# Kernel optimization log

Measured on AMD Instinct MI355X. Metric: run time of the kernel, lower is better.

The kernel has to match this reference:

```python
import jax, jax.numpy as jnp
import numpy as np

FEATURE_DIM = 2048
CROP_PE_DIM = 96
FULL = FEATURE_DIM + CROP_PE_DIM  # 2144
H1 = 1024
H2 = 512
NEG_SLOPE = 0.01


def leaky(x):
    return jnp.where(x >= 0, x, NEG_SLOPE * x)


def setup_inputs() -> dict:
    key = jax.random.key(0)
    ks = jax.random.split(key, 8)
    B, T = 512, 32
    features = jax.random.normal(ks[0], (B, T, FULL), dtype=jnp.float32)

    def lin(k, fan_in, fan_out):
        kw, kb = jax.random.split(k)
        bound = 1.0 / np.sqrt(fan_in)
        W = jax.random.uniform(kw, (fan_in, fan_out), minval=-bound, maxval=bound, dtype=jnp.float32)
        b = jax.random.uniform(kb, (fan_out,), minval=-bound, maxval=bound, dtype=jnp.float32)
        return W, b

    We, be = lin(ks[1], 2 * FULL, H1)
    W1a, b1a = lin(ks[2], H1, H1)
    W1b, b1b = lin(ks[3], H1, H2)
    W2a, b2a = lin(ks[4], H2, H2)
    W2b, b2b = lin(ks[5], H2, H2)
    Wd, bd = lin(ks[6], H2, 3)
    return {
        "features": features,
        "We": We, "be": be,
        "W1a": W1a, "b1a": b1a, "W1b": W1b, "b1b": b1b,
        "W2a": W2a, "b2a": b2a, "W2b": W2b, "b2b": b2b,
        "Wd": Wd, "bd": bd,
    }


def reference(features, We, be, W1a, b1a, W1b, b1b, W2a, b2a, W2b, b2b, Wd, bd):
    B, T, D = features.shape
    # Vectorized version of the double Python loop: pair each token with token 0.
    anchor = jnp.broadcast_to(features[:, :1, :], (B, T, D))  # features[i][0]
    features_full = jnp.concatenate((features, anchor), axis=-1).reshape(B * T, 2 * D)
    e_f = features_full @ We + be
    h = leaky(leaky(e_f) @ W1a + b1a)
    h = h @ W1b + b1b  # block1 output
    h2 = leaky(leaky(h) @ W2a + b2a) @ W2b + b2b  # block2
    h = h + h2
    translations = leaky(h) @ Wd + bd  # (B*T, 3)
    bias = jnp.array([[0.0, 0.0, 1.0]], dtype=translations.dtype)
    return translations + bias
```

## Files before the change

### kernel.cpp

```cpp
#include <hip/hip_runtime.h>
#include <hip/hip_bf16.h>
#include <stdint.h>

typedef __attribute__((ext_vector_type(4))) float f32x4;
typedef __attribute__((ext_vector_type(8))) short bf16x8;

#define BK 64

__device__ inline void gload_lds16(const void* g, void* l) {
    __builtin_amdgcn_global_load_lds(
        (const __attribute__((address_space(1))) void*)g,
        (__attribute__((address_space(3))) void*)l, 16, 0, 0);
}

__device__ inline void wg_barrier() {
    asm volatile("s_barrier" ::: "memory");
}
#define SCHED0 __builtin_amdgcn_sched_barrier(0)

__device__ inline int xcd_swizzle(int orig, int nwg) {
    int q = nwg >> 3, r = nwg & 7;
    int xcd = orig & 7, idx = orig >> 3;
    int base = (xcd < r) ? xcd * (q + 1) : r * (q + 1) + (xcd - r) * q;
    return base + idx;
}

__device__ inline float b2f(short s) {
    union { float f; unsigned u; } x; x.u = ((unsigned)(unsigned short)s) << 16; return x.f;
}
__device__ inline short f2bs(float f) {
    __hip_bfloat16 h = __float2bfloat16(f);
    short s; __builtin_memcpy(&s, &h, 2); return s;
}

__global__ __launch_bounds__(256) void cvt_feat(const float* __restrict__ in,
                                                __hip_bfloat16* __restrict__ out) {
    int i = blockIdx.x * 256 + threadIdx.x;
    const int CH = 16384 * 272;
    if (i >= CH) return;
    int r = i / 272, c8 = (i % 272) * 8;
    __hip_bfloat16 tmp[8];
    if (c8 < 2144) {
        const float4* p = (const float4*)(in + (size_t)r * 2144 + c8);
        float4 x0 = p[0], x1 = p[1];
        tmp[0] = __float2bfloat16(x0.x); tmp[1] = __float2bfloat16(x0.y);
        tmp[2] = __float2bfloat16(x0.z); tmp[3] = __float2bfloat16(x0.w);
        tmp[4] = __float2bfloat16(x1.x); tmp[5] = __float2bfloat16(x1.y);
        tmp[6] = __float2bfloat16(x1.z); tmp[7] = __float2bfloat16(x1.w);
    } else {
        #pragma unroll
        for (int j = 0; j < 8; j++) tmp[j] = __float2bfloat16(0.f);
    }
    *(bf16x8*)&out[(size_t)r * 2176 + c8] = *(const bf16x8*)tmp;
}

__global__ __launch_bounds__(256) void cvt_wt_t(const float* __restrict__ W,
                                                __hip_bfloat16* __restrict__ WT,
                                                int K, int N, int KP) {
    __shared__ float tile[32][33];
    const int ntn = N >> 5;
    const int tk = blockIdx.x / ntn, tn = blockIdx.x - tk * ntn;
    const int k0 = tk * 32, n0 = tn * 32;
    const int c = threadIdx.x & 31, r8 = threadIdx.x >> 5;
    #pragma unroll
    for (int p = 0; p < 4; p++) {
        int k = k0 + r8 + p * 8;
        tile[r8 + p * 8][c] = (k < K) ? W[(size_t)k * N + n0 + c] : 0.f;
    }
    __syncthreads();
    #pragma unroll
    for (int p = 0; p < 4; p++) {
        int n = n0 + r8 + p * 8;
        WT[(size_t)n * KP + k0 + c] = __float2bfloat16(tile[c][r8 + p * 8]);
    }
}

template<int BN_, int RES_MODE, int OUTK>
__global__ __launch_bounds__(512, 2)
void gemmk(const __hip_bfloat16* __restrict__ A, int lda,
           const __hip_bfloat16* __restrict__ Bt,
           const float* __restrict__ bias,
           const __hip_bfloat16* __restrict__ resb,
           const float* __restrict__ resf,
           __hip_bfloat16* __restrict__ outb,
           __hip_bfloat16* __restrict__ outb2,
           float* __restrict__ outf,
           int M, int N, int K, int gx)
{
    constexpr int NF  = BN_ / 64;
    constexpr int REL = NF * 16;
    __shared__ __hip_bfloat16 lds[2][(256 + BN_) * BK];

    const int nwg  = gridDim.x;
    const int wgid = xcd_swizzle(blockIdx.x, nwg);
    const int by   = wgid / gx;
    const int bx   = wgid - by * gx;

    const int t    = threadIdx.x;
    const int lane = t & 63;
    const int wv   = t >> 6;
    const int wr   = wv >> 2;
    const int wc   = wv & 3;

    const int row0 = by * 256;
    const int col0 = bx * BN_;

    const int NT = K / BK;
    const int split = blockIdx.y;
    const int kb = (split * NT) / gridDim.y;
    const int ke = ((split + 1) * NT) / gridDim.y;
    float* outfs = outf;
    if (OUTK == 0 && gridDim.y > 1) outfs = outf + (size_t)split * M * N;

    const int srow = t >> 3;
    const int sc8  = (t & 7) * 8;
    const int scol = sc8 ^ ((srow & 7) << 3);
    const int sdst = sc8;

    f32x4 acc[8][NF];
    #pragma unroll
    for (int i = 0; i < 8; i++)
        #pragma unroll
        for (int j = 0; j < NF; j++)
            acc[i][j] = f32x4{0.f, 0.f, 0.f, 0.f};

    const int lrow = lane & 15;
    const int lk   = (lane >> 4) * 8;
    const int rxor = (lrow & 7) << 3;

    auto stA_all = [&](int buf, int k0) {
        #pragma unroll
        for (int b = 0; b < 4; ++b)
            gload_lds16(A + (size_t)(row0 + b * 64 + srow) * lda + k0 + scol,
                        &lds[buf][(b * 64 + srow) * BK + sdst]);
    };
    auto stB_all = [&](int buf, int k0) {
        #pragma unroll
        for (int b = 0; b < NF; ++b)
            gload_lds16(Bt + (size_t)(col0 + b * 64 + srow) * K + k0 + scol,
                        &lds[buf][(256 + b * 64 + srow) * BK + sdst]);
    };

    bf16x8 bgall[NF][2];
    auto rdB_all = [&](int buf) {
        #pragma unroll
        for (int j = 0; j < NF; ++j)
            #pragma unroll
            for (int h = 0; h < 2; ++h)
                bgall[j][h] = *(const bf16x8*)
                    &lds[buf][(256 + wc * REL + j * 16 + lrow) * BK + ((h * 32 + lk) ^ rxor)];
    };
    bf16x8 af[4][2];
    auto rdA = [&](int buf, int ih) {
        #pragma unroll
        for (int i = 0; i < 4; ++i)
            #pragma unroll
            for (int h = 0; h < 2; ++h)
                af[i][h] = *(const bf16x8*)
                    &lds[buf][(wr * 128 + (ih * 4 + i) * 16 + lrow) * BK + ((h * 32 + lk) ^ rxor)];
    };

#define MFMA_Q(IB, JB)                                                        \
    do {                                                                      \
        __builtin_amdgcn_s_setprio(1);                                        \
        _Pragma("unroll") for (int h_ = 0; h_ < 2; ++h_)                      \
        _Pragma("unroll") for (int i_ = 0; i_ < 4; ++i_)                      \
        _Pragma("unroll") for (int j_ = 0; j_ < 2; ++j_)                      \
            acc[(IB) + i_][(JB) + j_] = __builtin_amdgcn_mfma_f32_16x16x32_bf16( \
                af[i_][h_], bgall[(JB) + j_][h_], acc[(IB) + i_][(JB) + j_], 0, 0, 0); \
        __builtin_amdgcn_s_setprio(0);                                        \
    } while (0)

    {
        const int k0 = kb * BK;
        stA_all(0, k0);
        stB_all(0, k0);
        asm volatile("s_waitcnt vmcnt(0)" ::: "memory");
        wg_barrier();
    }

    int cur = 0;
    for (int kt = kb; kt < ke; ++kt) {
        const bool pf = (kt + 1 < ke);
        const int nk0 = (kt + 1) * BK;
        if constexpr (NF == 4) {
            rdB_all(cur); rdA(cur, 0);
            if (pf) stA_all(cur ^ 1, nk0);
            wg_barrier(); SCHED0;
            MFMA_Q(0, 0);
            wg_barrier();
            if (pf) stB_all(cur ^ 1, nk0);
            wg_barrier(); SCHED0;
            MFMA_Q(0, 2);
            wg_barrier();
            rdA(cur, 1);
            wg_barrier(); SCHED0;
            MFMA_Q(4, 0);
            wg_barrier();
            MFMA_Q(4, 2);
            asm volatile("s_waitcnt vmcnt(0)" ::: "memory");
            wg_barrier();
        } else {
            rdB_all(cur); rdA(cur, 0);
            if (pf) { stA_all(cur ^ 1, nk0); stB_all(cur ^ 1, nk0); }
            wg_barrier(); SCHED0;
            MFMA_Q(0, 0);
            wg_barrier();
            rdA(cur, 1);
            wg_barrier(); SCHED0;
            MFMA_Q(4, 0);
            asm volatile("s_waitcnt vmcnt(0)" ::: "memory");
            wg_barrier();
        }
        cur ^= 1;
    }
#undef MFMA_Q

    if constexpr (OUTK == 0) {
        #pragma unroll
        for (int j = 0; j < NF; j++) {
            const int col = col0 + wc * REL + j * 16 + lrow;
            #pragma unroll
            for (int i = 0; i < 8; i++) {
                const int rbase = row0 + wr * 128 + i * 16 + (lane >> 4) * 4;
                #pragma unroll
                for (int r = 0; r < 4; r++)
                    outfs[(size_t)(rbase + r) * N + col] = acc[i][j][r];
            }
        }
    } else {
        wg_barrier();
        __hip_bfloat16* eb = &lds[0][0] + wv * (128 * REL);
        #pragma unroll
        for (int i = 0; i < 8; i++)
            #pragma unroll
            for (int j = 0; j < NF; j++)
                #pragma unroll
                for (int r = 0; r < 4; r++)
                    eb[(i * 16 + (lane >> 4) * 4 + r) * REL + j * 16 + lrow] =
                        __float2bfloat16(acc[i][j][r]);
        constexpr int LPR = REL / 8;
        constexpr int RPI = 64 / LPR;
        constexpr int NIT = 128 / RPI;
        const int lrr = lane / LPR;
        const int lcc = (lane % LPR) * 8;
        const int col = col0 + wc * REL + lcc;
        float bvv[8];
        if (bias) {
            float4 b0 = *(const float4*)&bias[col];
            float4 b1 = *(const float4*)&bias[col + 4];
            bvv[0] = b0.x; bvv[1] = b0.y; bvv[2] = b0.z; bvv[3] = b0.w;
            bvv[4] = b1.x; bvv[5] = b1.y; bvv[6] = b1.z; bvv[7] = b1.w;
        } else {
            #pragma unroll
            for (int e = 0; e < 8; e++) bvv[e] = 0.f;
        }
        #pragma unroll
        for (int it = 0; it < NIT; it++) {
            const int rl  = it * RPI + lrr;
            const int row = row0 + wr * 128 + rl;
            bf16x8 v8 = *(bf16x8*)&eb[rl * REL + lcc];
            float vv[8];
            #pragma unroll
            for (int e = 0; e < 8; e++) vv[e] = b2f(v8[e]) + bvv[e];
            if constexpr (RES_MODE == 1) {
                bf16x8 r8 = *(const bf16x8*)&resb[(size_t)row * N + col];
                #pragma unroll
                for (int e = 0; e < 8; e++) vv[e] += b2f(r8[e]);
            }
            if constexpr (RES_MODE == 2) {
                const float* rp = &resf[(size_t)(row >> 5) * N + col];
                float4 r0 = *(const float4*)rp;
                float4 r1 = *(const float4*)(rp + 4);
                vv[0] += r0.x; vv[1] += r0.y; vv[2] += r0.z; vv[3] += r0.w;
                vv[4] += r1.x; vv[5] += r1.y; vv[6] += r1.z; vv[7] += r1.w;
            }
            bf16x8 o1, o2;
            #pragma unroll
            for (int e = 0; e < 8; e++) {
                float lv = vv[e] >= 0.f ? vv[e] : 0.01f * vv[e];
                if constexpr (OUTK == 1) o1[e] = f2bs(lv);
                if constexpr (OUTK == 2) o1[e] = f2bs(vv[e]);
                if constexpr (OUTK == 3) { o1[e] = f2bs(lv); o2[e] = f2bs(vv[e]); }
            }
            *(bf16x8*)&outb[(size_t)row * N + col] = o1;
            if constexpr (OUTK == 3)
                *(bf16x8*)&outb2[(size_t)row * N + col] = o2;
        }
    }
}

__global__ __launch_bounds__(256)
void anchor_reduce(const float* __restrict__ part, const float* __restrict__ be,
                   float* __restrict__ out) {
    int i = blockIdx.x * 256 + threadIdx.x;
    if (i >= 512 * 1024) return;
    const int S = 512 * 1024;
    int col = i & 1023;
    float s = be[col];
    #pragma unroll
    for (int p = 0; p < 8; p++) s += part[i + p * S];
    out[i] = s;
}

__global__ __launch_bounds__(256)
void final_head(const __hip_bfloat16* __restrict__ h, const float* __restrict__ Wd,
                const float* __restrict__ bd, float* __restrict__ out)
{
    int row  = blockIdx.x * 4 + (threadIdx.x >> 6);
    int lane = threadIdx.x & 63;
    const __hip_bfloat16* hr = h + (size_t)row * 512;
    bf16x8 v8 = *(const bf16x8*)&hr[lane * 8];
    float s0 = 0.f, s1 = 0.f, s2 = 0.f;
    #pragma unroll
    for (int e = 0; e < 8; e++) {
        float v = b2f(v8[e]);
        v = v >= 0.f ? v : 0.01f * v;
        int k = lane * 8 + e;
        s0 += v * Wd[k * 3 + 0];
        s1 += v * Wd[k * 3 + 1];
        s2 += v * Wd[k * 3 + 2];
    }
    #pragma unroll
    for (int off = 32; off > 0; off >>= 1) {
        s0 += __shfl_down(s0, off);
        s1 += __shfl_down(s1, off);
        s2 += __shfl_down(s2, off);
    }
    if (lane == 0) {
        out[row * 3 + 0] = s0 + bd[0];
        out[row * 3 + 1] = s1 + bd[1];
        out[row * 3 + 2] = s2 + bd[2] + 1.0f;
    }
}

extern "C" void kernel_launch(void* const* d_in, const int* in_sizes, int n_in,
                              void* d_out, int out_size, void* d_ws, size_t ws_size,
                              hipStream_t stream)
{
    const float* features = (const float*)d_in[0];
    const float* We  = (const float*)d_in[1];
    const float* be  = (const float*)d_in[2];
    const float* W1a = (const float*)d_in[3];
    const float* b1a = (const float*)d_in[4];
    const float* W1b = (const float*)d_in[5];
    const float* b1b = (const float*)d_in[6];
    const float* W2a = (const float*)d_in[7];
    const float* b2a = (const float*)d_in[8];
    const float* W2b = (const float*)d_in[9];
    const float* b2b = (const float*)d_in[10];
    const float* Wd  = (const float*)d_in[11];
    const float* bd  = (const float*)d_in[12];
    float* out = (float*)d_out;

    char* ws = (char*)d_ws;
    size_t off = 0;
    auto alloc = [&](size_t bytes) -> char* {
        char* p = ws + off;
        off += (bytes + 255) & ~(size_t)255;
        return p;
    };
    __hip_bfloat16* featbf = (__hip_bfloat16*)alloc(16384ull * 2176 * 2);
    __hip_bfloat16* WeTt   = (__hip_bfloat16*)alloc(1024ull * 2176 * 2);
    __hip_bfloat16* WeTb   = (__hip_bfloat16*)alloc(1024ull * 2176 * 2);
    __hip_bfloat16* W1aT   = (__hip_bfloat16*)alloc(1024ull * 1024 * 2);
    __hip_bfloat16* W1bT   = (__hip_bfloat16*)alloc(512ull * 1024 * 2);
    __hip_bfloat16* W2aT   = (__hip_bfloat16*)alloc(512ull * 512 * 2);
    __hip_bfloat16* W2bT   = (__hip_bfloat16*)alloc(512ull * 512 * 2);
    float* eanchor_part    = (float*)alloc(8ull * 512 * 1024 * 4);
    float* eanchor         = (float*)alloc(512ull * 1024 * 4);
    char* bufA             = alloc(16384ull * 1024 * 2);
    char* bufB             = alloc(16384ull * 1024 * 2);
    __hip_bfloat16* h1b    = (__hip_bfloat16*)alloc(16384ull * 512 * 2);

    __hip_bfloat16* act1   = (__hip_bfloat16*)bufA;
    __hip_bfloat16* act2   = (__hip_bfloat16*)bufB;
    __hip_bfloat16* act3   = (__hip_bfloat16*)bufA;
    __hip_bfloat16* act4   = (__hip_bfloat16*)bufB;
    __hip_bfloat16* hsum_b = (__hip_bfloat16*)bufA;

    cvt_feat<<<(16384 * 272 + 255) / 256, 256, 0, stream>>>(features, featbf);
    cvt_wt_t<<<68 * 32, 256, 0, stream>>>(We,               WeTt, 2144, 1024, 2176);
    cvt_wt_t<<<68 * 32, 256, 0, stream>>>(We + 2144 * 1024, WeTb, 2144, 1024, 2176);
    cvt_wt_t<<<32 * 32, 256, 0, stream>>>(W1a, W1aT, 1024, 1024, 1024);
    cvt_wt_t<<<32 * 16, 256, 0, stream>>>(W1b, W1bT, 1024, 512, 1024);
    cvt_wt_t<<<16 * 16, 256, 0, stream>>>(W2a, W2aT, 512, 512, 512);
    cvt_wt_t<<<16 * 16, 256, 0, stream>>>(W2b, W2bT, 512, 512, 512);

    gemmk<256, 0, 0><<<dim3(8, 8), 512, 0, stream>>>(
        featbf, 32 * 2176, WeTb, nullptr, nullptr, nullptr,
        nullptr, nullptr, eanchor_part, 512, 1024, 2176, 4);
    anchor_reduce<<<2048, 256, 0, stream>>>(eanchor_part, be, eanchor);

    gemmk<256, 2, 1><<<dim3(256), 512, 0, stream>>>(
        featbf, 2176, WeTt, nullptr, nullptr, eanchor,
        act1, nullptr, nullptr, 16384, 1024, 2176, 4);

    gemmk<256, 0, 1><<<dim3(256), 512, 0, stream>>>(
        act1, 1024, W1aT, b1a, nullptr, nullptr,
        act2, nullptr, nullptr, 16384, 1024, 1024, 4);

    gemmk<128, 0, 3><<<dim3(256), 512, 0, stream>>>(
        act2, 1024, W1bT, b1b, nullptr, nullptr,
        act3, h1b, nullptr, 16384, 512, 1024, 4);

    gemmk<128, 0, 1><<<dim3(256), 512, 0, stream>>>(
        act3, 512, W2aT, b2a, nullptr, nullptr,
        act4, nullptr, nullptr, 16384, 512, 512, 4);

    gemmk<128, 1, 2><<<dim3(256), 512, 0, stream>>>(
        act4, 512, W2bT, b2b, h1b, nullptr,
        hsum_b, nullptr, nullptr, 16384, 512, 512, 4);

    final_head<<<4096, 256, 0, stream>>>(hsum_b, Wd, bd, out);
}
```

Baseline: 253.9 us.

## Deepen GEMM prefetch pipeline, merge prepass kernels, widen anchor split-K

The GEMM main loop now uses a split prefetch schedule. B tiles for the next step load into the other buffer, while A tiles for two steps ahead go into the current buffer once its A data has been read. Partial vmcnt waits replace the full drain at the end of each iteration, and the B fragments are read in two halves to cut register pressure. The seven conversion and transpose launches are merged into one prepass kernel, and the anchor split-K grows from 8 to 16 partitions with a matching reduce. This aims to hide global-load latency and cut launch overhead, at the cost of a more fragile wait and barrier ordering.

```diff
diff --git a/kernel.cpp b/kernel.cpp
--- a/kernel.cpp
+++ b/kernel.cpp
@@ -17,6 +17,7 @@
     asm volatile("s_barrier" ::: "memory");
 }
 #define SCHED0 __builtin_amdgcn_sched_barrier(0)
+#define VMW(n) asm volatile("s_waitcnt vmcnt(" #n ")" ::: "memory")
 
 __device__ inline int xcd_swizzle(int orig, int nwg) {
     int q = nwg >> 3, r = nwg & 7;
@@ -33,35 +34,13 @@
     short s; __builtin_memcpy(&s, &h, 2); return s;
 }
 
-__global__ __launch_bounds__(256) void cvt_feat(const float* __restrict__ in,
-                                                __hip_bfloat16* __restrict__ out) {
-    int i = blockIdx.x * 256 + threadIdx.x;
-    const int CH = 16384 * 272;
-    if (i >= CH) return;
-    int r = i / 272, c8 = (i % 272) * 8;
-    __hip_bfloat16 tmp[8];
-    if (c8 < 2144) {
-        const float4* p = (const float4*)(in + (size_t)r * 2144 + c8);
-        float4 x0 = p[0], x1 = p[1];
-        tmp[0] = __float2bfloat16(x0.x); tmp[1] = __float2bfloat16(x0.y);
-        tmp[2] = __float2bfloat16(x0.z); tmp[3] = __float2bfloat16(x0.w);
-        tmp[4] = __float2bfloat16(x1.x); tmp[5] = __float2bfloat16(x1.y);
-        tmp[6] = __float2bfloat16(x1.z); tmp[7] = __float2bfloat16(x1.w);
-    } else {
-        #pragma unroll
-        for (int j = 0; j < 8; j++) tmp[j] = __float2bfloat16(0.f);
-    }
-    *(bf16x8*)&out[(size_t)r * 2176 + c8] = *(const bf16x8*)tmp;
-}
-
-__global__ __launch_bounds__(256) void cvt_wt_t(const float* __restrict__ W,
-                                                __hip_bfloat16* __restrict__ WT,
-                                                int K, int N, int KP) {
+__device__ inline void wt_tile(const float* __restrict__ W, __hip_bfloat16* __restrict__ WT,
+                               int K, int N, int KP, int tid, int bid) {
     __shared__ float tile[32][33];
     const int ntn = N >> 5;
-    const int tk = blockIdx.x / ntn, tn = blockIdx.x - tk * ntn;
+    const int tk = bid / ntn, tn = bid - tk * ntn;
     const int k0 = tk * 32, n0 = tn * 32;
-    const int c = threadIdx.x & 31, r8 = threadIdx.x >> 5;
+    const int c = tid & 31, r8 = tid >> 5;
     #pragma unroll
     for (int p = 0; p < 4; p++) {
         int k = k0 + r8 + p * 8;
@@ -73,6 +52,44 @@
         int n = n0 + r8 + p * 8;
         WT[(size_t)n * KP + k0 + c] = __float2bfloat16(tile[c][r8 + p * 8]);
     }
+}
+
+__global__ __launch_bounds__(256)
+void prepass(const float* __restrict__ feat, __hip_bfloat16* __restrict__ featbf,
+             const float* __restrict__ We, __hip_bfloat16* __restrict__ WeTt,
+             __hip_bfloat16* __restrict__ WeTb,
+             const float* __restrict__ W1a, __hip_bfloat16* __restrict__ W1aT,
+             const float* __restrict__ W1b, __hip_bfloat16* __restrict__ W1bT,
+             const float* __restrict__ W2a, __hip_bfloat16* __restrict__ W2aT,
+             const float* __restrict__ W2b, __hip_bfloat16* __restrict__ W2bT)
+{
+    const int bid = blockIdx.x;
+    const int tid = threadIdx.x;
+    if (bid < 17408) {
+        int i = bid * 256 + tid;
+        int r = i / 272, c8 = (i % 272) * 8;
+        __hip_bfloat16 tmp[8];
+        if (c8 < 2144) {
+            const float4* p = (const float4*)(feat + (size_t)r * 2144 + c8);
+            float4 x0 = p[0], x1 = p[1];
+            tmp[0] = __float2bfloat16(x0.x); tmp[1] = __float2bfloat16(x0.y);
+            tmp[2] = __float2bfloat16(x0.z); tmp[3] = __float2bfloat16(x0.w);
+            tmp[4] = __float2bfloat16(x1.x); tmp[5] = __float2bfloat16(x1.y);
+            tmp[6] = __float2bfloat16(x1.z); tmp[7] = __float2bfloat16(x1.w);
+        } else {
+            #pragma unroll
+            for (int j = 0; j < 8; j++) tmp[j] = __float2bfloat16(0.f);
+        }
+        *(bf16x8*)&featbf[(size_t)r * 2176 + c8] = *(const bf16x8*)tmp;
+        return;
+    }
+    int b = bid - 17408;
+    if      (b < 2176) wt_tile(We,                WeTt, 2144, 1024, 2176, tid, b);
+    else if (b < 4352) wt_tile(We + 2144 * 1024,  WeTb, 2144, 1024, 2176, tid, b - 2176);
+    else if (b < 5376) wt_tile(W1a, W1aT, 1024, 1024, 1024, tid, b - 4352);
+    else if (b < 5888) wt_tile(W1b, W1bT, 1024,  512, 1024, tid, b - 5376);
+    else if (b < 6144) wt_tile(W2a, W2aT,  512,  512,  512, tid, b - 5888);
+    else               wt_tile(W2b, W2bT,  512,  512,  512, tid, b - 6144);
 }
 
 template<int BN_, int RES_MODE, int OUTK>
@@ -128,28 +145,15 @@
     const int lk   = (lane >> 4) * 8;
     const int rxor = (lrow & 7) << 3;
 
-    auto stA_all = [&](int buf, int k0) {
-        #pragma unroll
-        for (int b = 0; b < 4; ++b)
-            gload_lds16(A + (size_t)(row0 + b * 64 + srow) * lda + k0 + scol,
-                        &lds[buf][(b * 64 + srow) * BK + sdst]);
+    auto stA = [&](int buf, int k0, int b) {
+        gload_lds16(A + (size_t)(row0 + b * 64 + srow) * lda + k0 + scol,
+                    &lds[buf][(b * 64 + srow) * BK + sdst]);
     };
-    auto stB_all = [&](int buf, int k0) {
-        #pragma unroll
-        for (int b = 0; b < NF; ++b)
-            gload_lds16(Bt + (size_t)(col0 + b * 64 + srow) * K + k0 + scol,
-                        &lds[buf][(256 + b * 64 + srow) * BK + sdst]);
+    auto stB = [&](int buf, int k0, int b) {
+        gload_lds16(Bt + (size_t)(col0 + b * 64 + srow) * K + k0 + scol,
+                    &lds[buf][(256 + b * 64 + srow) * BK + sdst]);
     };
 
-    bf16x8 bgall[NF][2];
-    auto rdB_all = [&](int buf) {
-        #pragma unroll
-        for (int j = 0; j < NF; ++j)
-            #pragma unroll
-            for (int h = 0; h < 2; ++h)
-                bgall[j][h] = *(const bf16x8*)
-                    &lds[buf][(256 + wc * REL + j * 16 + lrow) * BK + ((h * 32 + lk) ^ rxor)];
-    };
     bf16x8 af[4][2];
     auto rdA = [&](int buf, int ih) {
         #pragma unroll
@@ -159,58 +163,79 @@
                 af[i][h] = *(const bf16x8*)
                     &lds[buf][(wr * 128 + (ih * 4 + i) * 16 + lrow) * BK + ((h * 32 + lk) ^ rxor)];
     };
-
-#define MFMA_Q(IB, JB)                                                        \
+    bf16x8 bgl[2][2], bgh[2][2];
+    auto rdB2 = [&](int buf, int jb, bf16x8 (&bg)[2][2]) {
+        #pragma unroll
+        for (int j = 0; j < 2; ++j)
+            #pragma unroll
+            for (int h = 0; h < 2; ++h)
+                bg[j][h] = *(const bf16x8*)
+                    &lds[buf][(256 + wc * REL + (jb + j) * 16 + lrow) * BK + ((h * 32 + lk) ^ rxor)];
+    };
+
+#define MFMA_Q(BG, IB, JB)                                                    \
     do {                                                                      \
         __builtin_amdgcn_s_setprio(1);                                        \
         _Pragma("unroll") for (int h_ = 0; h_ < 2; ++h_)                      \
         _Pragma("unroll") for (int i_ = 0; i_ < 4; ++i_)                      \
         _Pragma("unroll") for (int j_ = 0; j_ < 2; ++j_)                      \
             acc[(IB) + i_][(JB) + j_] = __builtin_amdgcn_mfma_f32_16x16x32_bf16( \
-                af[i_][h_], bgall[(JB) + j_][h_], acc[(IB) + i_][(JB) + j_], 0, 0, 0); \
+                af[i_][h_], BG[j_][h_], acc[(IB) + i_][(JB) + j_], 0, 0, 0);  \
         __builtin_amdgcn_s_setprio(0);                                        \
     } while (0)
 
     {
-        const int k0 = kb * BK;
-        stA_all(0, k0);
-        stB_all(0, k0);
-        asm volatile("s_waitcnt vmcnt(0)" ::: "memory");
-        wg_barrier();
+        const int k0 = kb * BK, k1 = (kb + 1) * BK;
+        if constexpr (NF == 4) {
+            stA(0, k0, 0); stA(0, k0, 2); stA(0, k0, 1); stA(0, k0, 3);
+            stB(0, k0, 0); stB(0, k0, 1); stB(0, k0, 2); stB(0, k0, 3);
+            stA(1, k1, 0); stA(1, k1, 2); stA(1, k1, 1); stA(1, k1, 3);
+        } else {
+            stA(0, k0, 0); stA(0, k0, 2); stB(0, k0, 0); stB(0, k0, 1);
+            stA(0, k0, 1); stA(0, k0, 3);
+            stA(1, k1, 0); stA(1, k1, 2); stB(1, k1, 0); stB(1, k1, 1);
+        }
     }
 
     int cur = 0;
     for (int kt = kb; kt < ke; ++kt) {
-        const bool pf = (kt + 1 < ke);
-        const int nk0 = (kt + 1) * BK;
+        const bool pf1 = (kt + 1 < ke), pf2 = (kt + 2 < ke);
+        const int nk1 = (kt + 1) * BK, nk2 = (kt + 2) * BK;
+        const int nxt = cur ^ 1;
         if constexpr (NF == 4) {
-            rdB_all(cur); rdA(cur, 0);
-            if (pf) stA_all(cur ^ 1, nk0);
-            wg_barrier(); SCHED0;
-            MFMA_Q(0, 0);
-            wg_barrier();
-            if (pf) stB_all(cur ^ 1, nk0);
-            wg_barrier(); SCHED0;
-            MFMA_Q(0, 2);
+            if (kt == ke - 1) VMW(0); else VMW(4);
+            wg_barrier();
+            rdA(cur, 0); rdB2(cur, 0, bgl);
+            if (pf1) { stB(nxt, nk1, 0); stB(nxt, nk1, 1); }
+            SCHED0;
+            MFMA_Q(bgl, 0, 0);
+            wg_barrier();
+            rdB2(cur, 2, bgh);
+            if (pf1) { stB(nxt, nk1, 2); stB(nxt, nk1, 3); }
+            SCHED0;
+            MFMA_Q(bgh, 0, 2);
             wg_barrier();
             rdA(cur, 1);
-            wg_barrier(); SCHED0;
-            MFMA_Q(4, 0);
-            wg_barrier();
-            MFMA_Q(4, 2);
-            asm volatile("s_waitcnt vmcnt(0)" ::: "memory");
-            wg_barrier();
+            if (pf2) { stA(cur, nk2, 0); stA(cur, nk2, 2); }
+            SCHED0;
+            MFMA_Q(bgl, 4, 0);
+            wg_barrier();
+            if (pf2) { stA(cur, nk2, 1); stA(cur, nk2, 3); }
+            SCHED0;
+            MFMA_Q(bgh, 4, 2);
         } else {
-            rdB_all(cur); rdA(cur, 0);
-            if (pf) { stA_all(cur ^ 1, nk0); stB_all(cur ^ 1, nk0); }
-            wg_barrier(); SCHED0;
-            MFMA_Q(0, 0);
+            if (kt == ke - 1) VMW(2); else VMW(6);
+            wg_barrier();
+            rdA(cur, 0); rdB2(cur, 0, bgl);
+            if (pf1) { stA(nxt, nk1, 1); stA(nxt, nk1, 3); }
+            SCHED0;
+            MFMA_Q(bgl, 0, 0);
+            if (kt == ke - 1) VMW(0); else VMW(6);
             wg_barrier();
             rdA(cur, 1);
-            wg_barrier(); SCHED0;
-            MFMA_Q(4, 0);
-            asm volatile("s_waitcnt vmcnt(0)" ::: "memory");
-            wg_barrier();
+            if (pf2) { stA(cur, nk2, 0); stA(cur, nk2, 2); stB(cur, nk2, 0); stB(cur, nk2, 1); }
+            SCHED0;
+            MFMA_Q(bgl, 4, 0);
         }
         cur ^= 1;
     }
@@ -299,7 +324,7 @@
     int col = i & 1023;
     float s = be[col];
     #pragma unroll
-    for (int p = 0; p < 8; p++) s += part[i + p * S];
+    for (int p = 0; p < 16; p++) s += part[i + p * S];
     out[i] = s;
 }
 
@@ -367,7 +392,7 @@
     __hip_bfloat16* W1bT   = (__hip_bfloat16*)alloc(512ull * 1024 * 2);
     __hip_bfloat16* W2aT   = (__hip_bfloat16*)alloc(512ull * 512 * 2);
     __hip_bfloat16* W2bT   = (__hip_bfloat16*)alloc(512ull * 512 * 2);
-    float* eanchor_part    = (float*)alloc(8ull * 512 * 1024 * 4);
+    float* eanchor_part    = (float*)alloc(16ull * 512 * 1024 * 4);
     float* eanchor         = (float*)alloc(512ull * 1024 * 4);
     char* bufA             = alloc(16384ull * 1024 * 2);
     char* bufB             = alloc(16384ull * 1024 * 2);
@@ -379,15 +404,10 @@
     __hip_bfloat16* act4   = (__hip_bfloat16*)bufB;
     __hip_bfloat16* hsum_b = (__hip_bfloat16*)bufA;
 
-    cvt_feat<<<(16384 * 272 + 255) / 256, 256, 0, stream>>>(features, featbf);
-    cvt_wt_t<<<68 * 32, 256, 0, stream>>>(We,               WeTt, 2144, 1024, 2176);
-    cvt_wt_t<<<68 * 32, 256, 0, stream>>>(We + 2144 * 1024, WeTb, 2144, 1024, 2176);
-    cvt_wt_t<<<32 * 32, 256, 0, stream>>>(W1a, W1aT, 1024, 1024, 1024);
-    cvt_wt_t<<<32 * 16, 256, 0, stream>>>(W1b, W1bT, 1024, 512, 1024);
-    cvt_wt_t<<<16 * 16, 256, 0, stream>>>(W2a, W2aT, 512, 512, 512);
-    cvt_wt_t<<<16 * 16, 256, 0, stream>>>(W2b, W2bT, 512, 512, 512);
-
-    gemmk<256, 0, 0><<<dim3(8, 8), 512, 0, stream>>>(
+    prepass<<<17408 + 6400, 256, 0, stream>>>(
+        features, featbf, We, WeTt, WeTb, W1a, W1aT, W1b, W1bT, W2a, W2aT, W2b, W2bT);
+
+    gemmk<256, 0, 0><<<dim3(8, 16), 512, 0, stream>>>(
         featbf, 32 * 2176, WeTb, nullptr, nullptr, nullptr,
         nullptr, nullptr, eanchor_part, 512, 1024, 2176, 4);
     anchor_reduce<<<2048, 256, 0, stream>>>(eanchor_part, be, eanchor);
```

After: 229.6 us. 9.6% less time.
